# Performance work log

Hardware: AMD Instinct MI355X
Metric: run time of the kernel (lower is better)

The kernel has to match this reference:

```python
import jax, jax.numpy as jnp
import numpy as np

EMBED_DIM = 256
NUM_HEADS = 8
N_Q = 300    # num queries
HW = 4096    # flattened key/value tokens
B = 16       # batch


def _linear(x, W, b):
    # torch nn.Linear: y = x @ W^T + b ; W is [out, in]
    return jnp.einsum('lbc,dc->lbd', x, W) + b


def setup_inputs() -> dict:
    key = jax.random.key(0)
    ks = jax.random.split(key, 32)
    C = EMBED_DIM
    s = 1.0 / np.sqrt(C)
    inp = {
        'query': jax.random.normal(ks[0], (N_Q, B, C), jnp.float32),
        'key': jax.random.normal(ks[1], (HW, B, C), jnp.float32),
        'value': jax.random.normal(ks[2], (HW, B, C), jnp.float32),
        'query_pos': jax.random.normal(ks[3], (N_Q, B, C), jnp.float32),
        'key_pos': jax.random.normal(ks[4], (HW, B, C), jnp.float32),
        'query_sine_embed': jax.random.normal(ks[5], (N_Q, B, C), jnp.float32),
    }
    names = ['qc', 'qp', 'qs', 'kc', 'kp', 'v', 'o']
    for i, nm in enumerate(names):
        inp[f'W_{nm}'] = jax.random.uniform(ks[6 + 2 * i], (C, C), jnp.float32, -s, s)
        inp[f'b_{nm}'] = jax.random.uniform(ks[7 + 2 * i], (C,), jnp.float32, -s, s)
    return inp


def reference(query, key, value, query_pos, key_pos, query_sine_embed,
              W_qc, b_qc, W_qp, b_qp, W_qs, b_qs, W_kc, b_kc,
              W_kp, b_kp, W_v, b_v, W_o, b_o):
    H = NUM_HEADS
    N, Bc, C = query.shape
    L = key.shape[0]
    Dh = C // H
    identity = query

    query_content = _linear(query, W_qc, b_qc)          # [N,B,C]
    key_content = _linear(key, W_kc, b_kc)              # [L,B,C]
    v = _linear(value, W_v, b_v)                        # [L,B,C]
    kp = _linear(key_pos, W_kp, b_kp)                   # [L,B,C]
    # is_first_layer == True branch
    qp = _linear(query_pos, W_qp, b_qp)                 # [N,B,C]
    q = query_content + qp
    k = key_content + kp

    qs = _linear(query_sine_embed, W_qs, b_qs)          # [N,B,C]
    # concat content and positional halves per head -> head dim 2*Dh
    q = jnp.concatenate([q.reshape(N, Bc, H, Dh), qs.reshape(N, Bc, H, Dh)], axis=3)
    k = jnp.concatenate([k.reshape(L, Bc, H, Dh), kp.reshape(L, Bc, H, Dh)], axis=3)

    q = q.transpose(1, 2, 0, 3)                          # [B,H,N,2Dh]
    k = k.transpose(1, 2, 0, 3)                          # [B,H,L,2Dh]
    v = v.reshape(L, Bc, H, Dh).transpose(1, 2, 0, 3)    # [B,H,L,Dh]

    scale = (2 * Dh) ** (-0.5)
    attn = jnp.einsum('bhnd,bhld->bhnl', q * scale, k)   # [B,H,N,L]
    attn = jax.nn.softmax(attn, axis=-1)
    out = jnp.einsum('bhnl,bhld->bhnd', attn, v)         # [B,H,N,Dh]
    out = out.transpose(0, 2, 1, 3).reshape(Bc, N, C)    # [B,N,C]
    out = jnp.einsum('bnc,dc->bnd', out, W_o) + b_o
    out = out.transpose(1, 0, 2)                         # [N,B,C]
    return identity + out
```

## Files before the change

### kernel.cpp

```cpp
#include <hip/hip_runtime.h>
#include <cstdint>
#include <cstddef>


typedef float  f4  __attribute__((ext_vector_type(4)));
typedef __bf16 b8v __attribute__((ext_vector_type(8)));

#define MFMA_BF16(a, b, c) __builtin_amdgcn_mfma_f32_16x16x32_bf16((a), (b), (c), 0, 0, 0)

#define GLD_LDS16(gp, lp)                                             \
  __builtin_amdgcn_global_load_lds(                                   \
      (const __attribute__((address_space(1))) void*)(gp),            \
      (__attribute__((address_space(3))) void*)(lp), 16, 0, 0)

#define KPLANE ((size_t)128 * 4096 * 32)

__global__ __launch_bounds__(256, 2) void key_side_gemm(
    const float* __restrict__ key, const float* __restrict__ key_pos,
    const float* __restrict__ value, const __bf16* __restrict__ Wbf,
    const float* __restrict__ b_kc, const float* __restrict__ b_kp,
    const float* __restrict__ b_v,
    __bf16* __restrict__ K64, __bf16* __restrict__ V32)
{
  __shared__ char smem[65536];
  const int tid  = threadIdx.x;
  const int wave = tid >> 6, lane = tid & 63;
  const int lrow = lane & 15, quad = lane >> 4;
  const int p  = blockIdx.y;
  const int lc = blockIdx.x >> 4;
  const int batch = blockIdx.x & 15;
  const int l0 = lc * 128;
  const int rowbase = (wave & 1) * 64;
  const int colbase = (wave >> 1) * 128;

  const float* __restrict__ X = (p == 0) ? key : (p == 1) ? key_pos : value;
  const __bf16* __restrict__ Wb = Wbf + (size_t)p * 65536;
  const float* __restrict__ bias = (p == 0) ? b_kc : (p == 1) ? b_kp : b_v;

  auto stageW = [&](int buf, int kc) {
#pragma unroll
    for (int it = 0; it < 8; ++it) {
      int slot = it * 256 + tid;
      int wr = slot >> 3, gp = slot & 7;
      int g  = gp ^ (wr & 7);
      GLD_LDS16(Wb + (size_t)wr * 256 + kc + g * 8, smem + buf * 32768 + slot * 16);
    }
  };
  auto readB = [&](int buf, int ct, int kk4) -> b8v {
    int wr = colbase + ct * 16 + lrow;
    int g  = (kk4 + quad) ^ (wr & 7);
    return *(const b8v*)(smem + buf * 32768 + wr * 128 + g * 16);
  };
  auto loadA = [&](float4* x0, float4* x1, int kc) {
#pragma unroll
    for (int rt = 0; rt < 4; ++rt) {
      const float* xp = X + ((size_t)(l0 + rowbase + rt * 16 + lrow) * 16 + batch) * 256
                          + kc + quad * 8;
      x0[rt] = *(const float4*)xp;
      x1[rt] = *(const float4*)(xp + 4);
    }
  };
  auto mk = [&](float4 x0, float4 x1) -> b8v {
    b8v t;
    t[0] = (__bf16)x0.x; t[1] = (__bf16)x0.y; t[2] = (__bf16)x0.z; t[3] = (__bf16)x0.w;
    t[4] = (__bf16)x1.x; t[5] = (__bf16)x1.y; t[6] = (__bf16)x1.z; t[7] = (__bf16)x1.w;
    return t;
  };

  f4 acc[4][8];
#pragma unroll
  for (int i = 0; i < 4; ++i)
#pragma unroll
    for (int j = 0; j < 8; ++j) acc[i][j] = f4{0.f, 0.f, 0.f, 0.f};

  float4 c0[4], c1[4], d0[4], d1[4];
  loadA(c0, c1, 0);
  stageW(0, 0);
  __syncthreads();

  for (int s = 0; s < 4; ++s) {
    const int kc0 = s * 64, buf = s & 1;
    loadA(d0, d1, kc0 + 32);
    if (s < 3) stageW(buf ^ 1, kc0 + 64);

    b8v a[4];
#pragma unroll
    for (int rt = 0; rt < 4; ++rt) a[rt] = mk(c0[rt], c1[rt]);
#pragma unroll
    for (int ct = 0; ct < 8; ++ct) {
      b8v bfr = readB(buf, ct, 0);
#pragma unroll
      for (int rt = 0; rt < 4; ++rt) acc[rt][ct] = MFMA_BF16(a[rt], bfr, acc[rt][ct]);
    }

    if (s < 3) loadA(c0, c1, kc0 + 64);

#pragma unroll
    for (int rt = 0; rt < 4; ++rt) a[rt] = mk(d0[rt], d1[rt]);
#pragma unroll
    for (int ct = 0; ct < 8; ++ct) {
      b8v bfr = readB(buf, ct, 4);
#pragma unroll
      for (int rt = 0; rt < 4; ++rt) acc[rt][ct] = MFMA_BF16(a[rt], bfr, acc[rt][ct]);
    }
    __syncthreads();
  }

  __bf16* Os = (__bf16*)smem;
#pragma unroll
  for (int ct = 0; ct < 8; ++ct) {
    int col = colbase + ct * 16 + lrow;
    float bv = bias[col];
    int cg = col >> 3, cr = col & 7;
#pragma unroll
    for (int rt = 0; rt < 4; ++rt)
#pragma unroll
      for (int r = 0; r < 4; ++r) {
        int row = rowbase + rt * 16 + quad * 4 + r;
        int g = cg ^ ((row ^ (row >> 3)) & 7);
        Os[row * 256 + g * 8 + cr] = (__bf16)(acc[rt][ct][r] + bv);
      }
  }
  __syncthreads();
#pragma unroll
  for (int it = 0; it < 16; ++it) {
    int h   = it >> 1;
    int row = (it & 1) * 64 + (tid >> 2);
    int seg = tid & 3;
    int g = (h * 4 + seg) ^ ((row ^ (row >> 3)) & 7);
    uint4 v = *(const uint4*)(Os + row * 256 + g * 8);
    size_t rowidx = ((size_t)(batch * 8 + h) * 4096) + l0 + row;
    if (p == 2) *(uint4*)(V32 + rowidx * 32 + seg * 8) = v;
    else        *(uint4*)(K64 + (size_t)p * KPLANE + rowidx * 32 + seg * 8) = v;
  }
}

__global__ __launch_bounds__(256) void query_conv(
    const float* __restrict__ query, const float* __restrict__ query_pos,
    const float* __restrict__ query_sine,
    const float* __restrict__ W_qc, const float* __restrict__ b_qc,
    const float* __restrict__ W_qp, const float* __restrict__ b_qp,
    const float* __restrict__ W_qs, const float* __restrict__ b_qs,
    __bf16* __restrict__ Q64,
    const float* __restrict__ W_kc, const float* __restrict__ W_kp,
    const float* __restrict__ W_v, __bf16* __restrict__ Wbf)
{
  __shared__ __bf16 Ws[256][72];
  if (blockIdx.x >= 75) {
    int i = (blockIdx.x - 75) * 256 + threadIdx.x;
    int base = i * 4;
    int m = base >> 16;
    int off = base & 65535;
    const float* W = (m == 0) ? W_kc : (m == 1) ? W_kp : W_v;
    float4 v = *(const float4*)(W + off);
    __bf16 o[4];
    o[0] = (__bf16)v.x; o[1] = (__bf16)v.y; o[2] = (__bf16)v.z; o[3] = (__bf16)v.w;
    *(uint2*)(Wbf + (size_t)m * 65536 + off) = *(uint2*)o;
    return;
  }
  const int tid  = threadIdx.x;
  const int wave = tid >> 6, lane = tid & 63;
  const int lrow = lane & 15, quad = lane >> 4;
  const int r0 = blockIdx.x * 64;

  f4 acc[16];
#pragma unroll
  for (int i = 0; i < 16; ++i) acc[i] = f4{0.f, 0.f, 0.f, 0.f};

  for (int kc = 0; kc < 768; kc += 64) {
    const float* X; const float* W;
    if (kc < 256)      { X = query;      W = W_qc; }
    else if (kc < 512) { X = query_pos;  W = W_qp; }
    else               { X = query_sine; W = W_qs; }
    const int ko = kc & 255;
#pragma unroll
    for (int it = 0; it < 16; ++it) {
      int idx = it * 256 + tid;
      int row = idx >> 4, c4 = idx & 15;
      float4 w = *(const float4*)(W + (size_t)row * 256 + ko + c4 * 4);
      __bf16* dp = &Ws[row][c4 * 4];
      dp[0] = (__bf16)w.x; dp[1] = (__bf16)w.y; dp[2] = (__bf16)w.z; dp[3] = (__bf16)w.w;
    }
    __syncthreads();
#pragma unroll
    for (int kk = 0; kk < 64; kk += 32) {
      const float* xp = X + (size_t)(r0 + wave * 16 + lrow) * 256 + ko + kk + quad * 8;
      float4 x0 = *(const float4*)xp;
      float4 x1 = *(const float4*)(xp + 4);
      b8v a;
      a[0] = (__bf16)x0.x; a[1] = (__bf16)x0.y; a[2] = (__bf16)x0.z; a[3] = (__bf16)x0.w;
      a[4] = (__bf16)x1.x; a[5] = (__bf16)x1.y; a[6] = (__bf16)x1.z; a[7] = (__bf16)x1.w;
#pragma unroll
      for (int ct = 0; ct < 16; ++ct) {
        b8v bf = *(const b8v*)&Ws[ct * 16 + lrow][kk + quad * 8];
        acc[ct] = MFMA_BF16(a, bf, acc[ct]);
      }
    }
    __syncthreads();
    if (kc == 448) {
#pragma unroll
      for (int ct = 0; ct < 16; ++ct) {
        int col = ct * 16 + lrow;
        float bsum = b_qc[col] + b_qp[col];
        int h = col >> 5, d = col & 31;
#pragma unroll
        for (int r = 0; r < 4; ++r) {
          int row = r0 + wave * 16 + quad * 4 + r;
          int n = row >> 4, bb = row & 15;
          Q64[((size_t)(bb * 8 + h) * 320 + n) * 64 + d] = (__bf16)((acc[ct][r] + bsum) * 0.125f);
        }
      }
    }
  }
#pragma unroll
  for (int ct = 0; ct < 16; ++ct) {
    int col = ct * 16 + lrow;
    float bsum = b_qc[col] + b_qp[col] + b_qs[col];
    int h = col >> 5, d = col & 31;
#pragma unroll
    for (int r = 0; r < 4; ++r) {
      int row = r0 + wave * 16 + quad * 4 + r;
      int n = row >> 4, bb = row & 15;
      Q64[((size_t)(bb * 8 + h) * 320 + n) * 64 + 32 + d] = (__bf16)((acc[ct][r] + bsum) * 0.125f);
    }
  }
}

__global__ __launch_bounds__(256, 2) void attn_part(
    const __bf16* __restrict__ Q64, const __bf16* __restrict__ K64,
    const __bf16* __restrict__ V32,
    __bf16* __restrict__ Opart, float* __restrict__ Mpart, float* __restrict__ Lpart)
{
  __shared__ __bf16 Ks[2][128 * 64];
  __shared__ __bf16 Vt[2][32][136];
  __shared__ __bf16 Pt[4][16][136];
  const int tid  = threadIdx.x;
  const int wave = tid >> 6, lane = tid & 63;
  const int lrow = lane & 15, quad = lane >> 4;
  const int ls = blockIdx.x, bh = blockIdx.y;
  const int l0base = ls * 1024;

  const __bf16* Kb0 = K64 + (size_t)bh * 4096 * 32;
  const __bf16* Kb1 = Kb0 + KPLANE;
  const __bf16* Vb  = V32 + (size_t)bh * 4096 * 32;

  b8v qa0[5], qa1[5];
#pragma unroll
  for (int t = 0; t < 5; ++t) {
    const __bf16* Qb = Q64 + ((size_t)bh * 320 + wave * 80 + t * 16 + lrow) * 64;
    qa0[t] = *(const b8v*)(Qb + quad * 8);
    qa1[t] = *(const b8v*)(Qb + 32 + quad * 8);
  }

  const int vs = tid & 3, vrh = tid >> 2;

  auto issueK = [&](int buf, int c) {
    int l0 = l0base + c * 128;
#pragma unroll
    for (int it = 0; it < 4; ++it) {
      int slot = it * 256 + tid, row = slot >> 3, gs = slot & 7;
      int g = gs ^ (row & 7);
      const __bf16* src = (g < 4)
          ? (Kb0 + (size_t)(l0 + row) * 32 + g * 8)
          : (Kb1 + (size_t)(l0 + row) * 32 + (g - 4) * 8);
      GLD_LDS16(src, (char*)&Ks[buf][0] + slot * 16);
    }
  };
  auto loadV = [&](uint4* vv, int c) {
    int l0 = l0base + c * 128;
    vv[0] = *(const uint4*)(Vb + (size_t)(l0 + 2 * vrh) * 32 + vs * 8);
    vv[1] = *(const uint4*)(Vb + (size_t)(l0 + 2 * vrh + 1) * 32 + vs * 8);
  };
  auto stageV = [&](int buf, const uint4* vv) {
    __bf16 a[8], b[8];
    *(uint4*)a = vv[0]; *(uint4*)b = vv[1];
#pragma unroll
    for (int j = 0; j < 8; ++j) {
      __bf16 pr[2] = {a[j], b[j]};
      *(uint32_t*)&Vt[buf][vs * 8 + j][2 * vrh] = *(const uint32_t*)pr;
    }
  };
  auto readKA = [&](int buf, int wr, int g) -> b8v {
    int gs = g ^ (wr & 7);
    return *(const b8v*)((const char*)&Ks[buf][0] + wr * 128 + gs * 16);
  };

  float mst[5], lst[5];
  f4 oacc[5][2];
#pragma unroll
  for (int t = 0; t < 5; ++t) {
    mst[t] = -1e30f; lst[t] = 0.f;
    oacc[t][0] = f4{0.f, 0.f, 0.f, 0.f};
    oacc[t][1] = f4{0.f, 0.f, 0.f, 0.f};
  }

  auto compute = [&](int buf) {
#pragma unroll
    for (int t = 0; t < 5; ++t) {
      f4 sc[8];
#pragma unroll
      for (int ct = 0; ct < 8; ++ct) {
        b8v ka0 = readKA(buf, ct * 16 + lrow, quad);
        b8v ka1 = readKA(buf, ct * 16 + lrow, 4 + quad);
        f4 z = f4{0.f, 0.f, 0.f, 0.f};
        z = MFMA_BF16(ka0, qa0[t], z);
        z = MFMA_BF16(ka1, qa1[t], z);
        sc[ct] = z;
      }
      float mx = sc[0][0];
#pragma unroll
      for (int ct = 0; ct < 8; ++ct)
#pragma unroll
        for (int r = 0; r < 4; ++r) mx = fmaxf(mx, sc[ct][r]);
      mx = fmaxf(mx, __shfl_xor(mx, 16));
      mx = fmaxf(mx, __shfl_xor(mx, 32));
      float mnew = fmaxf(mst[t], mx);
      float alpha = __expf(mst[t] - mnew);
      mst[t] = mnew;
      float rsum = 0.f;
#pragma unroll
      for (int ct = 0; ct < 8; ++ct)
#pragma unroll
        for (int r = 0; r < 4; ++r) {
          sc[ct][r] = __expf(sc[ct][r] - mnew);
          rsum += sc[ct][r];
        }
      rsum += __shfl_xor(rsum, 16);
      rsum += __shfl_xor(rsum, 32);
      lst[t] = lst[t] * alpha + rsum;
#pragma unroll
      for (int c2 = 0; c2 < 2; ++c2)
#pragma unroll
        for (int r = 0; r < 4; ++r) oacc[t][c2][r] *= alpha;

#pragma unroll
      for (int ct = 0; ct < 8; ++ct) {
        __bf16 p4[4];
#pragma unroll
        for (int r = 0; r < 4; ++r) p4[r] = (__bf16)sc[ct][r];
        *(uint2*)&Pt[wave][lrow][ct * 16 + quad * 4] = *(const uint2*)p4;
      }
#pragma unroll
      for (int kt = 0; kt < 4; ++kt) {
        b8v pb = *(const b8v*)&Pt[wave][lrow][kt * 32 + quad * 8];
#pragma unroll
        for (int c2 = 0; c2 < 2; ++c2) {
          b8v va = *(const b8v*)&Vt[buf][c2 * 16 + lrow][kt * 32 + quad * 8];
          oacc[t][c2] = MFMA_BF16(va, pb, oacc[t][c2]);
        }
      }
    }
  };

  uint4 vv[2];
  issueK(0, 0);
  loadV(vv, 0);
  for (int c = 0; c < 8; ++c) {
    const int cur = c & 1;
    stageV(cur, vv);
    __syncthreads();
    if (c + 1 < 8) {
      issueK(cur ^ 1, c + 1);
      loadV(vv, c + 1);
    }
    compute(cur);
  }

  const size_t pbase = ((size_t)bh * 4 + ls) * 320;
#pragma unroll
  for (int t = 0; t < 5; ++t) {
    int q = wave * 80 + t * 16 + lrow;
    float inv = 1.0f / lst[t];
#pragma unroll
    for (int c2 = 0; c2 < 2; ++c2) {
      __bf16 o4[4];
#pragma unroll
      for (int r = 0; r < 4; ++r) o4[r] = (__bf16)(oacc[t][c2][r] * inv);
      *(uint2*)&Opart[(pbase + q) * 32 + c2 * 16 + quad * 4] = *(const uint2*)o4;
    }
    if (quad == 0) {
      Mpart[pbase + q] = mst[t];
      Lpart[pbase + q] = lst[t];
    }
  }
}

__global__ __launch_bounds__(256) void attn_combine(
    const __bf16* __restrict__ Opart, const float* __restrict__ Mpart,
    const float* __restrict__ Lpart, __bf16* __restrict__ Obf)
{
  const int bh = blockIdx.y;
  const int idx = blockIdx.x * 256 + threadIdx.x;
  const int q = idx >> 5, d = idx & 31;
  if (q >= 300) return;
  const size_t rb = ((size_t)bh * 4) * 320 + q;
  float m0 = Mpart[rb], m1 = Mpart[rb + 320], m2 = Mpart[rb + 640], m3 = Mpart[rb + 960];
  float M = fmaxf(fmaxf(m0, m1), fmaxf(m2, m3));
  float w0 = Lpart[rb]       * __expf(m0 - M);
  float w1 = Lpart[rb + 320] * __expf(m1 - M);
  float w2 = Lpart[rb + 640] * __expf(m2 - M);
  float w3 = Lpart[rb + 960] * __expf(m3 - M);
  float S = w0 + w1 + w2 + w3;
  float o = w0 * (float)Opart[rb * 32 + d]
          + w1 * (float)Opart[(rb + 320) * 32 + d]
          + w2 * (float)Opart[(rb + 640) * 32 + d]
          + w3 * (float)Opart[(rb + 960) * 32 + d];
  int b = bh >> 3, h = bh & 7;
  Obf[((size_t)b * 300 + q) * 256 + h * 32 + d] = (__bf16)(o / S);
}

__global__ __launch_bounds__(256) void out_proj_gemm(
    const __bf16* __restrict__ Obf, const float* __restrict__ W_o,
    const float* __restrict__ b_o, const float* __restrict__ query,
    float* __restrict__ out)
{
  __shared__ __bf16 Ws[256][72];
  const int tid  = threadIdx.x;
  const int wave = tid >> 6, lane = tid & 63;
  const int lrow = lane & 15, quad = lane >> 4;
  const int r0 = blockIdx.x * 64;

  f4 acc[16];
#pragma unroll
  for (int i = 0; i < 16; ++i) acc[i] = f4{0.f, 0.f, 0.f, 0.f};

  for (int kc0 = 0; kc0 < 256; kc0 += 64) {
#pragma unroll
    for (int it = 0; it < 16; ++it) {
      int idx = it * 256 + tid;
      int row = idx >> 4, c4 = idx & 15;
      float4 w = *(const float4*)(W_o + (size_t)row * 256 + kc0 + c4 * 4);
      __bf16* dp = &Ws[row][c4 * 4];
      dp[0] = (__bf16)w.x; dp[1] = (__bf16)w.y; dp[2] = (__bf16)w.z; dp[3] = (__bf16)w.w;
    }
    __syncthreads();
#pragma unroll
    for (int kk = 0; kk < 64; kk += 32) {
      b8v a = *(const b8v*)(Obf + (size_t)(r0 + wave * 16 + lrow) * 256 + kc0 + kk + quad * 8);
#pragma unroll
      for (int ct = 0; ct < 16; ++ct) {
        b8v bf = *(const b8v*)&Ws[ct * 16 + lrow][kk + quad * 8];
        acc[ct] = MFMA_BF16(a, bf, acc[ct]);
      }
    }
    __syncthreads();
  }
#pragma unroll
  for (int ct = 0; ct < 16; ++ct) {
    int col = ct * 16 + lrow;
    float bo = b_o[col];
#pragma unroll
    for (int r = 0; r < 4; ++r) {
      int row = r0 + wave * 16 + quad * 4 + r;
      int bb = row / 300, n = row % 300;
      size_t oaddr = ((size_t)n * 16 + bb) * 256 + col;
      out[oaddr] = acc[ct][r] + bo + query[oaddr];
    }
  }
}

extern "C" void kernel_launch(void* const* d_in, const int* in_sizes, int n_in,
                              void* d_out, int out_size, void* d_ws, size_t ws_size,
                              hipStream_t stream) {
  (void)in_sizes; (void)n_in; (void)out_size; (void)ws_size;
  const float* query      = (const float*)d_in[0];
  const float* key        = (const float*)d_in[1];
  const float* value      = (const float*)d_in[2];
  const float* query_pos  = (const float*)d_in[3];
  const float* key_pos    = (const float*)d_in[4];
  const float* query_sine = (const float*)d_in[5];
  const float* W_qc = (const float*)d_in[6];  const float* b_qc = (const float*)d_in[7];
  const float* W_qp = (const float*)d_in[8];  const float* b_qp = (const float*)d_in[9];
  const float* W_qs = (const float*)d_in[10]; const float* b_qs = (const float*)d_in[11];
  const float* W_kc = (const float*)d_in[12]; const float* b_kc = (const float*)d_in[13];
  const float* W_kp = (const float*)d_in[14]; const float* b_kp = (const float*)d_in[15];
  const float* W_v  = (const float*)d_in[16]; const float* b_v  = (const float*)d_in[17];
  const float* W_o  = (const float*)d_in[18]; const float* b_o  = (const float*)d_in[19];
  float* out = (float*)d_out;

  char* ws = (char*)d_ws;
  constexpr size_t K64_BYTES = (size_t)128 * 4096 * 64 * 2;
  constexpr size_t V32_BYTES = (size_t)128 * 4096 * 32 * 2;
  constexpr size_t Q64_BYTES = (size_t)128 * 320 * 64 * 2;
  constexpr size_t OBF_BYTES = (size_t)16 * 300 * 256 * 2;
  constexpr size_t WBF_BYTES = (size_t)3 * 256 * 256 * 2;
  constexpr size_t OPART_BYTES = (size_t)128 * 4 * 320 * 32 * 2;
  constexpr size_t MPART_BYTES = (size_t)128 * 4 * 320 * 4;
  __bf16* K64 = (__bf16*)ws;
  __bf16* V32 = (__bf16*)(ws + K64_BYTES);
  __bf16* Q64 = (__bf16*)(ws + K64_BYTES + V32_BYTES);
  __bf16* Obf = (__bf16*)(ws + K64_BYTES + V32_BYTES + Q64_BYTES);
  __bf16* Wbf = (__bf16*)(ws + K64_BYTES + V32_BYTES + Q64_BYTES + OBF_BYTES);
  char*  pbase = ws + K64_BYTES + V32_BYTES + Q64_BYTES + OBF_BYTES + WBF_BYTES;
  __bf16* Opart = (__bf16*)pbase;
  float*  Mpart = (float*)(pbase + OPART_BYTES);
  float*  Lpart = (float*)(pbase + OPART_BYTES + MPART_BYTES);

  hipLaunchKernelGGL(query_conv, dim3(267), dim3(256), 0, stream,
                     query, query_pos, query_sine, W_qc, b_qc, W_qp, b_qp, W_qs, b_qs, Q64,
                     W_kc, W_kp, W_v, Wbf);
  hipLaunchKernelGGL(key_side_gemm, dim3(512, 3), dim3(256), 0, stream,
                     key, key_pos, value, Wbf, b_kc, b_kp, b_v, K64, V32);
  hipLaunchKernelGGL(attn_part, dim3(4, 128), dim3(256), 0, stream,
                     Q64, K64, V32, Opart, Mpart, Lpart);
  hipLaunchKernelGGL(attn_combine, dim3(40, 128), dim3(256), 0, stream,
                     Opart, Mpart, Lpart, Obf);
  hipLaunchKernelGGL(out_proj_gemm, dim3(75), dim3(256), 0, stream,
                     Obf, W_o, b_o, query, out);
}
```

Baseline: 401.1 us.

## Shrink key-side GEMM tile to 64 rows and read weights directly from global

The key/key_pos/value projection GEMM now uses 64-row tiles instead of 128, doubling the grid, and each wave computes a 64x64 output slice. The double-buffered LDS staging of weights via global_load_lds and its per-stage barriers are removed; each wave reads bf16 weight fragments straight from global/L2. The aim is more blocks, smaller register footprint and higher occupancy for a memory-bound fp32 input stream, at the cost of less weight reuse through LDS and no explicit load/compute software pipelining.

Result: slower. 463.0 us (+15.4%).

```diff
diff --git a/kernel.cpp b/kernel.cpp
--- a/kernel.cpp
+++ b/kernel.cpp
@@ -22,110 +22,79 @@
     const float* __restrict__ b_v,
     __bf16* __restrict__ K64, __bf16* __restrict__ V32)
 {
-  __shared__ char smem[65536];
+  __shared__ __bf16 Os[64 * 256];
   const int tid  = threadIdx.x;
   const int wave = tid >> 6, lane = tid & 63;
   const int lrow = lane & 15, quad = lane >> 4;
   const int p  = blockIdx.y;
   const int lc = blockIdx.x >> 4;
   const int batch = blockIdx.x & 15;
-  const int l0 = lc * 128;
-  const int rowbase = (wave & 1) * 64;
-  const int colbase = (wave >> 1) * 128;
+  const int l0 = lc * 64;
+  const int wavecol = wave * 64;
 
   const float* __restrict__ X = (p == 0) ? key : (p == 1) ? key_pos : value;
   const __bf16* __restrict__ Wb = Wbf + (size_t)p * 65536;
   const float* __restrict__ bias = (p == 0) ? b_kc : (p == 1) ? b_kp : b_v;
 
-  auto stageW = [&](int buf, int kc) {
-#pragma unroll
-    for (int it = 0; it < 8; ++it) {
-      int slot = it * 256 + tid;
-      int wr = slot >> 3, gp = slot & 7;
-      int g  = gp ^ (wr & 7);
-      GLD_LDS16(Wb + (size_t)wr * 256 + kc + g * 8, smem + buf * 32768 + slot * 16);
-    }
-  };
-  auto readB = [&](int buf, int ct, int kk4) -> b8v {
-    int wr = colbase + ct * 16 + lrow;
-    int g  = (kk4 + quad) ^ (wr & 7);
-    return *(const b8v*)(smem + buf * 32768 + wr * 128 + g * 16);
-  };
-  auto loadA = [&](float4* x0, float4* x1, int kc) {
+  f4 acc[4][4];
+#pragma unroll
+  for (int i = 0; i < 4; ++i)
+#pragma unroll
+    for (int j = 0; j < 4; ++j) acc[i][j] = f4{0.f, 0.f, 0.f, 0.f};
+
+  const float* xb[4];
+  const __bf16* wb[4];
+#pragma unroll
+  for (int rt = 0; rt < 4; ++rt)
+    xb[rt] = X + ((size_t)(l0 + rt * 16 + lrow) * 16 + batch) * 256 + quad * 8;
+#pragma unroll
+  for (int ct = 0; ct < 4; ++ct)
+    wb[ct] = Wb + (size_t)(wavecol + ct * 16 + lrow) * 256 + quad * 8;
+
+#pragma unroll 2
+  for (int s = 0; s < 8; ++s) {
+    const int kc = s * 32;
+    float4 x0[4], x1[4];
 #pragma unroll
     for (int rt = 0; rt < 4; ++rt) {
-      const float* xp = X + ((size_t)(l0 + rowbase + rt * 16 + lrow) * 16 + batch) * 256
-                          + kc + quad * 8;
-      x0[rt] = *(const float4*)xp;
-      x1[rt] = *(const float4*)(xp + 4);
-    }
-  };
-  auto mk = [&](float4 x0, float4 x1) -> b8v {
-    b8v t;
-    t[0] = (__bf16)x0.x; t[1] = (__bf16)x0.y; t[2] = (__bf16)x0.z; t[3] = (__bf16)x0.w;
-    t[4] = (__bf16)x1.x; t[5] = (__bf16)x1.y; t[6] = (__bf16)x1.z; t[7] = (__bf16)x1.w;
-    return t;
-  };
-
-  f4 acc[4][8];
-#pragma unroll
-  for (int i = 0; i < 4; ++i)
-#pragma unroll
-    for (int j = 0; j < 8; ++j) acc[i][j] = f4{0.f, 0.f, 0.f, 0.f};
-
-  float4 c0[4], c1[4], d0[4], d1[4];
-  loadA(c0, c1, 0);
-  stageW(0, 0);
-  __syncthreads();
-
-  for (int s = 0; s < 4; ++s) {
-    const int kc0 = s * 64, buf = s & 1;
-    loadA(d0, d1, kc0 + 32);
-    if (s < 3) stageW(buf ^ 1, kc0 + 64);
-
-    b8v a[4];
-#pragma unroll
-    for (int rt = 0; rt < 4; ++rt) a[rt] = mk(c0[rt], c1[rt]);
-#pragma unroll
-    for (int ct = 0; ct < 8; ++ct) {
-      b8v bfr = readB(buf, ct, 0);
-#pragma unroll
-      for (int rt = 0; rt < 4; ++rt) acc[rt][ct] = MFMA_BF16(a[rt], bfr, acc[rt][ct]);
-    }
-
-    if (s < 3) loadA(c0, c1, kc0 + 64);
-
-#pragma unroll
-    for (int rt = 0; rt < 4; ++rt) a[rt] = mk(d0[rt], d1[rt]);
-#pragma unroll
-    for (int ct = 0; ct < 8; ++ct) {
-      b8v bfr = readB(buf, ct, 4);
-#pragma unroll
-      for (int rt = 0; rt < 4; ++rt) acc[rt][ct] = MFMA_BF16(a[rt], bfr, acc[rt][ct]);
-    }
-    __syncthreads();
-  }
-
-  __bf16* Os = (__bf16*)smem;
-#pragma unroll
-  for (int ct = 0; ct < 8; ++ct) {
-    int col = colbase + ct * 16 + lrow;
+      x0[rt] = *(const float4*)(xb[rt] + kc);
+      x1[rt] = *(const float4*)(xb[rt] + kc + 4);
+    }
+    b8v bf[4];
+#pragma unroll
+    for (int ct = 0; ct < 4; ++ct)
+      bf[ct] = *(const b8v*)(wb[ct] + kc);
+#pragma unroll
+    for (int rt = 0; rt < 4; ++rt) {
+      b8v a;
+      a[0] = (__bf16)x0[rt].x; a[1] = (__bf16)x0[rt].y;
+      a[2] = (__bf16)x0[rt].z; a[3] = (__bf16)x0[rt].w;
+      a[4] = (__bf16)x1[rt].x; a[5] = (__bf16)x1[rt].y;
+      a[6] = (__bf16)x1[rt].z; a[7] = (__bf16)x1[rt].w;
+#pragma unroll
+      for (int ct = 0; ct < 4; ++ct)
+        acc[rt][ct] = MFMA_BF16(a, bf[ct], acc[rt][ct]);
+    }
+  }
+
+#pragma unroll
+  for (int ct = 0; ct < 4; ++ct) {
+    int col = wavecol + ct * 16 + lrow;
     float bv = bias[col];
     int cg = col >> 3, cr = col & 7;
 #pragma unroll
     for (int rt = 0; rt < 4; ++rt)
 #pragma unroll
       for (int r = 0; r < 4; ++r) {
-        int row = rowbase + rt * 16 + quad * 4 + r;
+        int row = rt * 16 + quad * 4 + r;
         int g = cg ^ ((row ^ (row >> 3)) & 7);
         Os[row * 256 + g * 8 + cr] = (__bf16)(acc[rt][ct][r] + bv);
       }
   }
   __syncthreads();
 #pragma unroll
-  for (int it = 0; it < 16; ++it) {
-    int h   = it >> 1;
-    int row = (it & 1) * 64 + (tid >> 2);
+  for (int h = 0; h < 8; ++h) {
+    int row = tid >> 2;
     int seg = tid & 3;
     int g = (h * 4 + seg) ^ ((row ^ (row >> 3)) & 7);
     uint4 v = *(const uint4*)(Os + row * 256 + g * 8);
@@ -499,7 +468,7 @@
   hipLaunchKernelGGL(query_conv, dim3(267), dim3(256), 0, stream,
                      query, query_pos, query_sine, W_qc, b_qc, W_qp, b_qp, W_qs, b_qs, Q64,
                      W_kc, W_kp, W_v, Wbf);
-  hipLaunchKernelGGL(key_side_gemm, dim3(512, 3), dim3(256), 0, stream,
+  hipLaunchKernelGGL(key_side_gemm, dim3(1024, 3), dim3(256), 0, stream,
                      key, key_pos, value, Wbf, b_kc, b_kp, b_v, K64, V32);
   hipLaunchKernelGGL(attn_part, dim3(4, 128), dim3(256), 0, stream,
                      Q64, K64, V32, Opart, Mpart, Lpart);
```

## Split key-side GEMM into column halves and merge query projection into it

Applied to the files above, without the earlier changes.

The key/value projection GEMM now computes 128 output columns per block instead of 256, doubling the grid to 3072 blocks and halving LDS use to 36KB. The aim is better occupancy and wave balance across CUs. The query projection runs as extra blocks (x >= 1024, y == 0) inside the same launch, so it overlaps with the key-side work. Weight conversion moves into its own small kernel that runs first. In exchange, the X activation rows are read twice (once per column half), the grid carries 150 idle early-exit blocks, and there is still one extra launch.

After: 445.9 us. 1.11x slower.

```diff
diff --git a/kernel.cpp b/kernel.cpp
--- a/kernel.cpp
+++ b/kernel.cpp
@@ -15,23 +15,116 @@
 
 #define KPLANE ((size_t)128 * 4096 * 32)
 
-__global__ __launch_bounds__(256, 2) void key_side_gemm(
+__global__ __launch_bounds__(256) void convert_w(
+    const float* __restrict__ W0, const float* __restrict__ W1,
+    const float* __restrict__ W2, __bf16* __restrict__ Wbf)
+{
+  int i = blockIdx.x * 256 + threadIdx.x;
+  int base = i * 4;
+  int m = base >> 16;
+  int off = base & 65535;
+  const float* W = (m == 0) ? W0 : (m == 1) ? W1 : W2;
+  float4 v = *(const float4*)(W + off);
+  __bf16 o[4];
+  o[0] = (__bf16)v.x; o[1] = (__bf16)v.y; o[2] = (__bf16)v.z; o[3] = (__bf16)v.w;
+  *(uint2*)(Wbf + (size_t)m * 65536 + off) = *(uint2*)o;
+}
+
+__global__ __launch_bounds__(256, 2) void proj_gemm(
     const float* __restrict__ key, const float* __restrict__ key_pos,
     const float* __restrict__ value, const __bf16* __restrict__ Wbf,
     const float* __restrict__ b_kc, const float* __restrict__ b_kp,
     const float* __restrict__ b_v,
-    __bf16* __restrict__ K64, __bf16* __restrict__ V32)
+    __bf16* __restrict__ K64, __bf16* __restrict__ V32,
+    const float* __restrict__ query, const float* __restrict__ query_pos,
+    const float* __restrict__ query_sine,
+    const float* __restrict__ W_qc, const float* __restrict__ b_qc,
+    const float* __restrict__ W_qp, const float* __restrict__ b_qp,
+    const float* __restrict__ W_qs, const float* __restrict__ b_qs,
+    __bf16* __restrict__ Q64)
 {
-  __shared__ char smem[65536];
+  __shared__ char smem[36864];
   const int tid  = threadIdx.x;
   const int wave = tid >> 6, lane = tid & 63;
   const int lrow = lane & 15, quad = lane >> 4;
+
+  if (blockIdx.x >= 1024) {
+    if (blockIdx.y != 0) return;
+    const int r0 = (blockIdx.x - 1024) * 64;
+    __bf16 (*Ws)[72] = (__bf16(*)[72])smem;
+
+    f4 acc[16];
+#pragma unroll
+    for (int i = 0; i < 16; ++i) acc[i] = f4{0.f, 0.f, 0.f, 0.f};
+
+    for (int kc = 0; kc < 768; kc += 64) {
+      const float* X; const float* W;
+      if (kc < 256)      { X = query;      W = W_qc; }
+      else if (kc < 512) { X = query_pos;  W = W_qp; }
+      else               { X = query_sine; W = W_qs; }
+      const int ko = kc & 255;
+#pragma unroll
+      for (int it = 0; it < 16; ++it) {
+        int idx = it * 256 + tid;
+        int row = idx >> 4, c4 = idx & 15;
+        float4 w = *(const float4*)(W + (size_t)row * 256 + ko + c4 * 4);
+        __bf16* dp = &Ws[row][c4 * 4];
+        dp[0] = (__bf16)w.x; dp[1] = (__bf16)w.y; dp[2] = (__bf16)w.z; dp[3] = (__bf16)w.w;
+      }
+      __syncthreads();
+#pragma unroll
+      for (int kk = 0; kk < 64; kk += 32) {
+        const float* xp = X + (size_t)(r0 + wave * 16 + lrow) * 256 + ko + kk + quad * 8;
+        float4 x0 = *(const float4*)xp;
+        float4 x1 = *(const float4*)(xp + 4);
+        b8v a;
+        a[0] = (__bf16)x0.x; a[1] = (__bf16)x0.y; a[2] = (__bf16)x0.z; a[3] = (__bf16)x0.w;
+        a[4] = (__bf16)x1.x; a[5] = (__bf16)x1.y; a[6] = (__bf16)x1.z; a[7] = (__bf16)x1.w;
+#pragma unroll
+        for (int ct = 0; ct < 16; ++ct) {
+          b8v bf = *(const b8v*)&Ws[ct * 16 + lrow][kk + quad * 8];
+          acc[ct] = MFMA_BF16(a, bf, acc[ct]);
+        }
+      }
+      __syncthreads();
+      if (kc == 448) {
+#pragma unroll
+        for (int ct = 0; ct < 16; ++ct) {
+          int col = ct * 16 + lrow;
+          float bsum = b_qc[col] + b_qp[col];
+          int h = col >> 5, d = col & 31;
+#pragma unroll
+          for (int r = 0; r < 4; ++r) {
+            int row = r0 + wave * 16 + quad * 4 + r;
+            int n = row >> 4, bb = row & 15;
+            Q64[((size_t)(bb * 8 + h) * 320 + n) * 64 + d] = (__bf16)((acc[ct][r] + bsum) * 0.125f);
+          }
+        }
+      }
+    }
+#pragma unroll
+    for (int ct = 0; ct < 16; ++ct) {
+      int col = ct * 16 + lrow;
+      float bsum = b_qc[col] + b_qp[col] + b_qs[col];
+      int h = col >> 5, d = col & 31;
+#pragma unroll
+      for (int r = 0; r < 4; ++r) {
+        int row = r0 + wave * 16 + quad * 4 + r;
+        int n = row >> 4, bb = row & 15;
+        Q64[((size_t)(bb * 8 + h) * 320 + n) * 64 + 32 + d] = (__bf16)((acc[ct][r] + bsum) * 0.125f);
+      }
+    }
+    return;
+  }
+
   const int p  = blockIdx.y;
-  const int lc = blockIdx.x >> 4;
   const int batch = blockIdx.x & 15;
+  const int lc = (blockIdx.x >> 4) & 31;
+  const int ch = blockIdx.x >> 9;
   const int l0 = lc * 128;
+  const int col0 = ch * 128;
   const int rowbase = (wave & 1) * 64;
-  const int colbase = (wave >> 1) * 128;
+  const int colbase = (wave >> 1) * 64;
 
   const float* __restrict__ X = (p == 0) ? key : (p == 1) ? key_pos : value;
   const __bf16* __restrict__ Wb = Wbf + (size_t)p * 65536;
@@ -39,17 +132,18 @@
 
   auto stageW = [&](int buf, int kc) {
 #pragma unroll
-    for (int it = 0; it < 8; ++it) {
+    for (int it = 0; it < 4; ++it) {
       int slot = it * 256 + tid;
       int wr = slot >> 3, gp = slot & 7;
       int g  = gp ^ (wr & 7);
-      GLD_LDS16(Wb + (size_t)wr * 256 + kc + g * 8, smem + buf * 32768 + slot * 16);
+      GLD_LDS16(Wb + (size_t)(col0 + wr) * 256 + kc + g * 8,
+                smem + buf * 16384 + slot * 16);
     }
   };
   auto readB = [&](int buf, int ct, int kk4) -> b8v {
     int wr = colbase + ct * 16 + lrow;
     int g  = (kk4 + quad) ^ (wr & 7);
-    return *(const b8v*)(smem + buf * 32768 + wr * 128 + g * 16);
+    return *(const b8v*)(smem + buf * 16384 + wr * 128 + g * 16);
   };
   auto loadA = [&](float4* x0, float4* x1, int kc) {
 #pragma unroll
@@ -67,11 +161,11 @@
     return t;
   };
 
-  f4 acc[4][8];
+  f4 acc[4][4];
 #pragma unroll
   for (int i = 0; i < 4; ++i)
 #pragma unroll
-    for (int j = 0; j < 8; ++j) acc[i][j] = f4{0.f, 0.f, 0.f, 0.f};
+    for (int j = 0; j < 4; ++j) acc[i][j] = f4{0.f, 0.f, 0.f, 0.f};
 
   float4 c0[4], c1[4], d0[4], d1[4];
   loadA(c0, c1, 0);
@@ -87,7 +181,7 @@
 #pragma unroll
     for (int rt = 0; rt < 4; ++rt) a[rt] = mk(c0[rt], c1[rt]);
 #pragma unroll
-    for (int ct = 0; ct < 8; ++ct) {
+    for (int ct = 0; ct < 4; ++ct) {
       b8v bfr = readB(buf, ct, 0);
 #pragma unroll
       for (int rt = 0; rt < 4; ++rt) acc[rt][ct] = MFMA_BF16(a[rt], bfr, acc[rt][ct]);
@@ -98,7 +192,7 @@
 #pragma unroll
     for (int rt = 0; rt < 4; ++rt) a[rt] = mk(d0[rt], d1[rt]);
 #pragma unroll
-    for (int ct = 0; ct < 8; ++ct) {
+    for (int ct = 0; ct < 4; ++ct) {
       b8v bfr = readB(buf, ct, 4);
 #pragma unroll
       for (int rt = 0; rt < 4; ++rt) acc[rt][ct] = MFMA_BF16(a[rt], bfr, acc[rt][ct]);
@@ -108,9 +202,9 @@
 
   __bf16* Os = (__bf16*)smem;
 #pragma unroll
-  for (int ct = 0; ct < 8; ++ct) {
+  for (int ct = 0; ct < 4; ++ct) {
     int col = colbase + ct * 16 + lrow;
-    float bv = bias[col];
+    float bv = bias[col0 + col];
     int cg = col >> 3, cr = col & 7;
 #pragma unroll
     for (int rt = 0; rt < 4; ++rt)
@@ -118,111 +212,21 @@
       for (int r = 0; r < 4; ++r) {
         int row = rowbase + rt * 16 + quad * 4 + r;
         int g = cg ^ ((row ^ (row >> 3)) & 7);
-        Os[row * 256 + g * 8 + cr] = (__bf16)(acc[rt][ct][r] + bv);
+        Os[row * 128 + g * 8 + cr] = (__bf16)(acc[rt][ct][r] + bv);
       }
   }
   __syncthreads();
 #pragma unroll
-  for (int it = 0; it < 16; ++it) {
-    int h   = it >> 1;
+  for (int it = 0; it < 8; ++it) {
+    int hh  = it >> 1;
     int row = (it & 1) * 64 + (tid >> 2);
     int seg = tid & 3;
-    int g = (h * 4 + seg) ^ ((row ^ (row >> 3)) & 7);
-    uint4 v = *(const uint4*)(Os + row * 256 + g * 8);
+    int g = (hh * 4 + seg) ^ ((row ^ (row >> 3)) & 7);
+    uint4 v = *(const uint4*)(Os + row * 128 + g * 8);
+    int h = ch * 4 + hh;
     size_t rowidx = ((size_t)(batch * 8 + h) * 4096) + l0 + row;
     if (p == 2) *(uint4*)(V32 + rowidx * 32 + seg * 8) = v;
     else        *(uint4*)(K64 + (size_t)p * KPLANE + rowidx * 32 + seg * 8) = v;
-  }
-}
-
-__global__ __launch_bounds__(256) void query_conv(
-    const float* __restrict__ query, const float* __restrict__ query_pos,
-    const float* __restrict__ query_sine,
-    const float* __restrict__ W_qc, const float* __restrict__ b_qc,
-    const float* __restrict__ W_qp, const float* __restrict__ b_qp,
-    const float* __restrict__ W_qs, const float* __restrict__ b_qs,
-    __bf16* __restrict__ Q64,
-    const float* __restrict__ W_kc, const float* __restrict__ W_kp,
-    const float* __restrict__ W_v, __bf16* __restrict__ Wbf)
-{
-  __shared__ __bf16 Ws[256][72];
-  if (blockIdx.x >= 75) {
-    int i = (blockIdx.x - 75) * 256 + threadIdx.x;
-    int base = i * 4;
-    int m = base >> 16;
-    int off = base & 65535;
-    const float* W = (m == 0) ? W_kc : (m == 1) ? W_kp : W_v;
-    float4 v = *(const float4*)(W + off);
-    __bf16 o[4];
-    o[0] = (__bf16)v.x; o[1] = (__bf16)v.y; o[2] = (__bf16)v.z; o[3] = (__bf16)v.w;
-    *(uint2*)(Wbf + (size_t)m * 65536 + off) = *(uint2*)o;
-    return;
-  }
-  const int tid  = threadIdx.x;
-  const int wave = tid >> 6, lane = tid & 63;
-  const int lrow = lane & 15, quad = lane >> 4;
-  const int r0 = blockIdx.x * 64;
-
-  f4 acc[16];
-#pragma unroll
-  for (int i = 0; i < 16; ++i) acc[i] = f4{0.f, 0.f, 0.f, 0.f};
-
-  for (int kc = 0; kc < 768; kc += 64) {
-    const float* X; const float* W;
-    if (kc < 256)      { X = query;      W = W_qc; }
-    else if (kc < 512) { X = query_pos;  W = W_qp; }
-    else               { X = query_sine; W = W_qs; }
-    const int ko = kc & 255;
-#pragma unroll
-    for (int it = 0; it < 16; ++it) {
-      int idx = it * 256 + tid;
-      int row = idx >> 4, c4 = idx & 15;
-      float4 w = *(const float4*)(W + (size_t)row * 256 + ko + c4 * 4);
-      __bf16* dp = &Ws[row][c4 * 4];
-      dp[0] = (__bf16)w.x; dp[1] = (__bf16)w.y; dp[2] = (__bf16)w.z; dp[3] = (__bf16)w.w;
-    }
-    __syncthreads();
-#pragma unroll
-    for (int kk = 0; kk < 64; kk += 32) {
-      const float* xp = X + (size_t)(r0 + wave * 16 + lrow) * 256 + ko + kk + quad * 8;
-      float4 x0 = *(const float4*)xp;
-      float4 x1 = *(const float4*)(xp + 4);
-      b8v a;
-      a[0] = (__bf16)x0.x; a[1] = (__bf16)x0.y; a[2] = (__bf16)x0.z; a[3] = (__bf16)x0.w;
-      a[4] = (__bf16)x1.x; a[5] = (__bf16)x1.y; a[6] = (__bf16)x1.z; a[7] = (__bf16)x1.w;
-#pragma unroll
-      for (int ct = 0; ct < 16; ++ct) {
-        b8v bf = *(const b8v*)&Ws[ct * 16 + lrow][kk + quad * 8];
-        acc[ct] = MFMA_BF16(a, bf, acc[ct]);
-      }
-    }
-    __syncthreads();
-    if (kc == 448) {
-#pragma unroll
-      for (int ct = 0; ct < 16; ++ct) {
-        int col = ct * 16 + lrow;
-        float bsum = b_qc[col] + b_qp[col];
-        int h = col >> 5, d = col & 31;
-#pragma unroll
-        for (int r = 0; r < 4; ++r) {
-          int row = r0 + wave * 16 + quad * 4 + r;
-          int n = row >> 4, bb = row & 15;
-          Q64[((size_t)(bb * 8 + h) * 320 + n) * 64 + d] = (__bf16)((acc[ct][r] + bsum) * 0.125f);
-        }
-      }
-    }
-  }
-#pragma unroll
-  for (int ct = 0; ct < 16; ++ct) {
-    int col = ct * 16 + lrow;
-    float bsum = b_qc[col] + b_qp[col] + b_qs[col];
-    int h = col >> 5, d = col & 31;
-#pragma unroll
-    for (int r = 0; r < 4; ++r) {
-      int row = r0 + wave * 16 + quad * 4 + r;
-      int n = row >> 4, bb = row & 15;
-      Q64[((size_t)(bb * 8 + h) * 320 + n) * 64 + 32 + d] = (__bf16)((acc[ct][r] + bsum) * 0.125f);
-    }
   }
 }
 
@@ -496,11 +500,12 @@
   float*  Mpart = (float*)(pbase + OPART_BYTES);
   float*  Lpart = (float*)(pbase + OPART_BYTES + MPART_BYTES);
 
-  hipLaunchKernelGGL(query_conv, dim3(267), dim3(256), 0, stream,
-                     query, query_pos, query_sine, W_qc, b_qc, W_qp, b_qp, W_qs, b_qs, Q64,
+  hipLaunchKernelGGL(convert_w, dim3(192), dim3(256), 0, stream,
                      W_kc, W_kp, W_v, Wbf);
-  hipLaunchKernelGGL(key_side_gemm, dim3(512, 3), dim3(256), 0, stream,
-                     key, key_pos, value, Wbf, b_kc, b_kp, b_v, K64, V32);
+  hipLaunchKernelGGL(proj_gemm, dim3(1099, 3), dim3(256), 0, stream,
+                     key, key_pos, value, Wbf, b_kc, b_kp, b_v, K64, V32,
+                     query, query_pos, query_sine,
+                     W_qc, b_qc, W_qp, b_qp, W_qs, b_qs, Q64);
   hipLaunchKernelGGL(attn_part, dim3(4, 128), dim3(256), 0, stream,
                      Q64, K64, V32, Opart, Mpart, Lpart);
   hipLaunchKernelGGL(attn_combine, dim3(40, 128), dim3(256), 0, stream,
```
